# Performance work log

Measured on AMD Instinct MI355X. Metric: run time of the kernel, lower is better.

The kernel has to match this reference:

```python
import jax, jax.numpy as jnp
import numpy as np

HID, H, C, L = 128, 4, 128, 3  # hidden, heads, per-head out (concat=False -> mean over heads), layers
OUT = 256
N_HEX, N_VERT, N_EDGE, B = 19, 54, 72, 1024
F_HEX, F_VERT, F_EDGE, F_PLY = 9, 7, 5, 14


def _topology():
    # Deterministic stand-in for the Catan board topology (same edge counts as the env).
    rng = np.random.RandomState(0)
    hv = rng.randint(0, N_VERT, size=(N_HEX, 6))            # each hex touches 6 vertices
    v0 = rng.randint(0, N_VERT, size=N_EDGE)                # board-edge endpoints
    v1 = (v0 + 1 + rng.randint(0, N_VERT - 1, size=N_EDGE)) % N_VERT
    h_src = np.repeat(np.arange(N_HEX), 6); h_dst = hv.reshape(-1)           # 114 edges
    e_src = np.repeat(np.arange(N_EDGE), 2); e_dst = np.stack([v0, v1], 1).reshape(-1)  # 144
    vv_s = np.concatenate([v0, v1]); vv_d = np.concatenate([v1, v0])          # 144
    # (src_idx, dst_idx, n_dst) per relation, order matches RELATION_TYPES
    rels = [(h_src, h_dst, N_VERT),   # hex -> vertex
            (h_dst, h_src, N_HEX),    # vertex -> hex
            (e_dst, e_src, N_EDGE),   # vertex -> edge
            (e_src, e_dst, N_VERT),   # edge -> vertex
            (vv_s, vv_d, N_VERT)]     # vertex -> vertex
    return [(jnp.asarray(s, jnp.int32), jnp.asarray(d, jnp.int32), nd) for s, d, nd in rels]

RELS = _topology()
REL_TYPES = [("hex", "vertex"), ("vertex", "hex"), ("vertex", "edge"), ("edge", "vertex"), ("vertex", "vertex")]
NODE_TYPES = ("hex", "vertex", "edge")


def _gat(x_src, x_dst, W, a_s, a_d, b, src, dst, n_dst):
    """PyG GATConv (heads=H, concat=False, add_self_loops=False, shared lin)."""
    bsz = x_src.shape[0]
    g = (x_src @ W).reshape(bsz, -1, H, C)    # [B,Ns,H,C]
    gd = (x_dst @ W).reshape(bsz, -1, H, C)   # [B,Nd,H,C]
    es = jnp.einsum('bnhc,hc->bnh', g, a_s)
    ed = jnp.einsum('bnhc,hc->bnh', gd, a_d)
    e = jax.nn.leaky_relu(es[:, src] + ed[:, dst], 0.2)   # [B,E,H]
    e = jnp.transpose(e, (1, 0, 2))                       # [E,B,H]
    m = jax.ops.segment_max(e, dst, num_segments=n_dst)   # per-dst softmax
    ex = jnp.exp(e - m[dst])
    s = jax.ops.segment_sum(ex, dst, num_segments=n_dst)
    alpha = ex / (s[dst] + 1e-16)
    msg = jnp.transpose(g, (1, 0, 2, 3))[src] * alpha[..., None]   # [E,B,H,C]
    out = jax.ops.segment_sum(msg, dst, num_segments=n_dst)       # [Nd,B,H,C]
    return jnp.transpose(out.mean(axis=2), (1, 0, 2)) + b         # mean over heads, + bias


def _ln(x, g, b):
    mu = x.mean(-1, keepdims=True)
    var = ((x - mu) ** 2).mean(-1, keepdims=True)
    return (x - mu) / jnp.sqrt(var + 1e-5) * g + b


def setup_inputs() -> dict:
    key = jax.random.key(0)
    ks = jax.random.split(key, 20)
    rn = lambda k, shape, s=0.05: jax.random.normal(k, shape, jnp.float32) * s
    pool_dim = 3 * HID + F_PLY
    return {
        'hex_features': rn(ks[0], (B, N_HEX, F_HEX), 1.0),
        'vertex_features': rn(ks[1], (B, N_VERT, F_VERT), 1.0),
        'edge_features': rn(ks[2], (B, N_EDGE, F_EDGE), 1.0),
        'player_features': rn(ks[3], (B, 4, F_PLY), 1.0),
        'in_hexW': rn(ks[4], (F_HEX, HID)), 'in_hexb': jnp.zeros((HID,), jnp.float32),
        'in_vertW': rn(ks[5], (F_VERT, HID)), 'in_vertb': jnp.zeros((HID,), jnp.float32),
        'in_edgeW': rn(ks[6], (F_EDGE, HID)), 'in_edgeb': jnp.zeros((HID,), jnp.float32),
        'gat_W': rn(ks[7], (L, 5, HID, H * C)),
        'gat_asrc': rn(ks[8], (L, 5, H, C)),
        'gat_adst': rn(ks[9], (L, 5, H, C)),
        'gat_b': jnp.zeros((L, 5, C), jnp.float32),
        'ln_g': jnp.ones((L, 3, HID), jnp.float32),
        'ln_b': jnp.zeros((L, 3, HID), jnp.float32),
        'mlp_W1': rn(ks[10], (pool_dim, HID)), 'mlp_b1': jnp.zeros((HID,), jnp.float32),
        'mlp_W2': rn(ks[11], (HID, OUT)), 'mlp_b2': jnp.zeros((OUT,), jnp.float32),
        'current_player': jax.random.randint(ks[12], (B,), 0, 4, jnp.int32),
    }


def reference(hex_features, vertex_features, edge_features, player_features,
              in_hexW, in_hexb, in_vertW, in_vertb, in_edgeW, in_edgeb,
              gat_W, gat_asrc, gat_adst, gat_b, ln_g, ln_b,
              mlp_W1, mlp_b1, mlp_W2, mlp_b2, current_player):
    x = {'hex': hex_features @ in_hexW + in_hexb,
         'vertex': vertex_features @ in_vertW + in_vertb,
         'edge': edge_features @ in_edgeW + in_edgeb}
    for l in range(L):
        agg = {nt: jnp.zeros_like(x[nt]) for nt in NODE_TYPES}
        for r, (st, dt) in enumerate(REL_TYPES):
            src, dst, n_dst = RELS[r]
            agg[dt] = agg[dt] + _gat(x[st], x[dt], gat_W[l, r], gat_asrc[l, r],
                                     gat_adst[l, r], gat_b[l, r], src, dst, n_dst)
        for i, nt in enumerate(NODE_TYPES):
            x[nt] = jax.nn.relu(_ln(agg[nt] + x[nt], ln_g[l, i], ln_b[l, i]))
    pools = [x[nt].mean(axis=1) for nt in NODE_TYPES]  # mean-pool each node type
    cur = jnp.take_along_axis(player_features, current_player[:, None, None], axis=1)[:, 0]
    feat = jnp.concatenate(pools + [cur], axis=-1)     # [B, 3*HID + F_PLY]
    h = jax.nn.relu(feat @ mlp_W1 + mlp_b1)
    return h @ mlp_W2 + mlp_b2
```

## Files before the change

### kernel.cpp

```cpp
#include <hip/hip_runtime.h>
#include <math.h>

#define NB 1024
#define NHEX 19
#define NVERT 54
#define NEDGE 72
#define NNODE 145
#define HID 128
#define NLAYERS 3
#define MAXE 144
#define OUTD 256
#define FPLY 14
#define POOLD 398
#define ESD_PB 5120

typedef unsigned short ushort_t;
typedef short bf16x8 __attribute__((ext_vector_type(8)));
typedef float f32x4 __attribute__((ext_vector_type(4)));
typedef float f32x2 __attribute__((ext_vector_type(2)));

static __device__ __forceinline__ float bf2f(ushort_t u) {
    return __uint_as_float(((unsigned int)u) << 16);
}
static __device__ __forceinline__ ushort_t f2bf(float f) {
    unsigned int u = __float_as_uint(f);
    return (ushort_t)((u + 0x7fffu + ((u >> 16) & 1u)) >> 16);
}
static __device__ __forceinline__ unsigned pk2(float lo, float hi) {
    unsigned r;
    asm("v_cvt_pk_bf16_f32 %0, %1, %2" : "=v"(r) : "v"(lo), "v"(hi));
    return r;
}
static __device__ __forceinline__ float blo(unsigned u) { return __uint_as_float(u << 16); }
static __device__ __forceinline__ float bhi(unsigned u) { return __uint_as_float(u & 0xffff0000u); }
static __device__ __forceinline__ f32x4 MF(uint4 a, uint4 b, f32x4 c) {
    return __builtin_amdgcn_mfma_f32_16x16x32_bf16(
        __builtin_bit_cast(bf16x8, a), __builtin_bit_cast(bf16x8, b), c, 0, 0, 0);
}
static __device__ __forceinline__ int xba(int row, int cb) {
    return (row * 256 + cb) ^ ((row & 7) << 4);
}

__device__ __forceinline__ void topo_body(int* __restrict__ cst_g, unsigned* __restrict__ pck_g) {
    __shared__ unsigned mt[624];
    __shared__ int t6[624];
    __shared__ int sc[624];
    __shared__ int hv[114], v0a[72], v1a[72];
    __shared__ int cnt[80];
    __shared__ int dloc[73 * 24];
    __shared__ int J186;
    const int tid = threadIdx.x;

    if (tid == 0) {
        unsigned s = 0u;
        for (int i = 0; i < 624; ++i) { mt[i] = s; s = 1812433253u * (s ^ (s >> 30)) + (unsigned)i + 1u; }
    }
    __syncthreads();
    {
        unsigned a = 0, bb = 0, c = 0;
        if (tid < 227) { a = mt[tid]; bb = mt[tid + 1]; c = mt[tid + 397]; }
        __syncthreads();
        if (tid < 227) {
            unsigned y = (a & 0x80000000u) | (bb & 0x7fffffffu);
            mt[tid] = c ^ (y >> 1) ^ ((bb & 1u) ? 0x9908b0dfu : 0u);
        }
        __syncthreads();
    }
    {
        int i = 227 + tid;
        unsigned a = 0, bb = 0, c = 0;
        if (tid < 227) { a = mt[i]; bb = mt[i + 1]; c = mt[i - 227]; }
        __syncthreads();
        if (tid < 227) {
            unsigned y = (a & 0x80000000u) | (bb & 0x7fffffffu);
            mt[i] = c ^ (y >> 1) ^ ((bb & 1u) ? 0x9908b0dfu : 0u);
        }
        __syncthreads();
    }
    {
        int i = 454 + tid;
        unsigned a = 0, bb = 0, c = 0;
        if (tid < 170) { a = mt[i]; bb = mt[(i + 1) % 624]; c = mt[i - 227]; }
        __syncthreads();
        if (tid < 170) {
            unsigned y = (a & 0x80000000u) | (bb & 0x7fffffffu);
            mt[i] = c ^ (y >> 1) ^ ((bb & 1u) ? 0x9908b0dfu : 0u);
        }
        __syncthreads();
    }
    for (int i = tid; i < 624; i += 256) {
        unsigned y = mt[i];
        y ^= y >> 11; y ^= (y << 7) & 0x9d2c5680u; y ^= (y << 15) & 0xefc60000u; y ^= y >> 18;
        t6[i] = (int)(y & 63u);
    }
    __syncthreads();
#define SCAN624()                                                          \
    for (int off = 1; off < 624; off <<= 1) {                              \
        int v0_ = 0, v1_ = 0, v2_ = 0;                                     \
        int i0 = tid, i1 = tid + 256, i2 = tid + 512;                      \
        if (i0 >= off) v0_ = sc[i0 - off];                                 \
        if (i1 >= off) v1_ = sc[i1 - off];                                 \
        if (i2 < 624 && i2 >= off) v2_ = sc[i2 - off];                     \
        __syncthreads();                                                   \
        sc[i0] += v0_; sc[i1] += v1_;                                      \
        if (i2 < 624) sc[i2] += v2_;                                       \
        __syncthreads();                                                   \
    }
    for (int i = tid; i < 624; i += 256) sc[i] = (t6[i] <= 53) ? 1 : 0;
    __syncthreads();
    SCAN624();
    for (int i = tid; i < 624; i += 256) {
        if (t6[i] <= 53) {
            int k = sc[i];
            if (k <= 114) hv[k - 1] = t6[i];
            else if (k <= 186) v0a[k - 115] = t6[i];
            if (k == 186) J186 = i;
        }
    }
    __syncthreads();
    int Jcap = J186;
    for (int i = tid; i < 624; i += 256) sc[i] = (i > Jcap && t6[i] <= 52) ? 1 : 0;
    __syncthreads();
    SCAN624();
    for (int i = tid; i < 624; i += 256) {
        if (i > Jcap && t6[i] <= 52) {
            int k = sc[i];
            if (k <= 72) v1a[k - 1] = (v0a[k - 1] + 1 + t6[i]) % 54;
        }
    }
    __syncthreads();
#undef SCAN624
    const int En[5] = {114, 114, 144, 144, 144};
    const int Ndn[5] = {54, 19, 72, 54, 54};
    for (int r = 0; r < 5; ++r) {
        int E = En[r], Nd = Ndn[r];
        int myc = 0;
        if (tid < Nd) {
            int* ss = dloc + tid * 24;
            for (int k = 0; k < E; ++k) {
                int s, d;
                if (r == 0)      { s = k / 6; d = hv[k]; }
                else if (r == 1) { s = hv[k]; d = k / 6; }
                else if (r == 2) { s = (k & 1) ? v1a[k >> 1] : v0a[k >> 1]; d = k >> 1; }
                else if (r == 3) { s = k >> 1; d = (k & 1) ? v1a[k >> 1] : v0a[k >> 1]; }
                else             { s = (k < 72) ? v0a[k] : v1a[k - 72]; d = (k < 72) ? v1a[k] : v0a[k - 72]; }
                if (d != tid) continue;
                int f = -1;
                for (int i2 = 0; i2 < myc; ++i2) if ((ss[i2] & 255) == s) { f = i2; break; }
                if (f >= 0) ss[f] += 1 << 16;
                else { if (myc < 24) { ss[myc++] = s | (1 << 16); } }
            }
            cnt[tid] = myc;
        }
        __syncthreads();
        for (int off = 1; off < 128; off <<= 1) {
            int v = 0;
            if (tid < Nd && tid >= off) v = cnt[tid - off];
            __syncthreads();
            if (tid < Nd && tid >= off) cnt[tid] += v;
            __syncthreads();
        }
        if (tid < Nd) {
            int st = cnt[tid] - myc;
            cst_g[r * 73 + tid] = st;
            if (tid == Nd - 1) cst_g[r * 73 + Nd] = cnt[tid];
            int* ss = dloc + tid * 24;
            for (int i2 = 0; i2 < myc; ++i2)
                pck_g[r * 144 + st + i2] =
                    (unsigned)((ss[i2] & 255) | (tid << 8) | ((ss[i2] >> 16) << 16));
        }
        __syncthreads();
    }
}

__device__ __forceinline__ void wvec_body(int lr, const float* __restrict__ gat_W,
                                          const float* __restrict__ gat_asrc,
                                          const float* __restrict__ gat_adst,
                                          ushort_t* __restrict__ wvb) {
    __shared__ float as_s[512], ad_s[512];
    int tid = threadIdx.x;
    for (int i = tid; i < 512; i += 256) {
        as_s[i] = gat_asrc[(size_t)lr * 512 + i];
        ad_s[i] = gat_adst[(size_t)lr * 512 + i];
    }
    __syncthreads();
    ushort_t* wb = wvb + (size_t)lr * 2048;
    const float* W = gat_W + (size_t)lr * 128 * 512;
    int t127 = tid & 127, rhalf = tid >> 7;
    int h = t127 >> 5, c4 = t127 & 31;
    for (int k0 = 0; k0 < 128; k0 += 2) {
        int k = k0 + rhalf;
        float4 wv4 = *(const float4*)(W + (size_t)k * 512 + h * 128 + c4 * 4);
        const float* a = as_s + h * 128 + c4 * 4;
        const float* dd = ad_s + h * 128 + c4 * 4;
        float pa = wv4.x * a[0] + wv4.y * a[1] + wv4.z * a[2] + wv4.w * a[3];
        float pd = wv4.x * dd[0] + wv4.y * dd[1] + wv4.z * dd[2] + wv4.w * dd[3];
        for (int m = 1; m < 32; m <<= 1) { pa += __shfl_xor(pa, m, 64); pd += __shfl_xor(pd, m, 64); }
        if (c4 == 0) {
            ushort_t pah = f2bf(pa), pdh = f2bf(pd);
            ushort_t pal = f2bf(pa - bf2f(pah)), pdl = f2bf(pd - bf2f(pdh));
            wb[h * 128 + k] = pah;        wb[(4 + h) * 128 + k] = pdh;
            wb[(8 + h) * 128 + k] = pal;  wb[(12 + h) * 128 + k] = pdl;
        }
    }
}

__device__ __forceinline__ void wp_body(int lrh, const float* __restrict__ gat_W, ushort_t* __restrict__ Wp) {
    __shared__ ushort_t tr[128 * 130];
    int lr = lrh >> 2, h = lrh & 3;
    const float* Wsrc = gat_W + (size_t)lr * 128 * 512 + h * 128;
    for (int i = threadIdx.x; i < 128 * 32; i += 256) {
        int k = i >> 5, q = i & 31;
        float4 v = *(const float4*)(Wsrc + (size_t)k * 512 + q * 4);
        int n = q * 4;
        tr[(n + 0) * 130 + k] = f2bf(v.x);
        tr[(n + 1) * 130 + k] = f2bf(v.y);
        tr[(n + 2) * 130 + k] = f2bf(v.z);
        tr[(n + 3) * 130 + k] = f2bf(v.w);
    }
    __syncthreads();
    ushort_t* dst = Wp + (size_t)lrh * 128 * 128;
    for (int i = threadIdx.x; i < 128 * 16; i += 256) {
        int n = i >> 4, q = i & 15;
        const ushort_t* s = tr + n * 130 + q * 8;
        uint4 o;
        o.x = (unsigned)s[0] | ((unsigned)s[1] << 16);
        o.y = (unsigned)s[2] | ((unsigned)s[3] << 16);
        o.z = (unsigned)s[4] | ((unsigned)s[5] << 16);
        o.w = (unsigned)s[6] | ((unsigned)s[7] << 16);
        *(uint4*)(dst + n * 128 + q * 8) = o;
    }
}

__device__ __forceinline__ void proj_body(int b, const float* __restrict__ hexf, const float* __restrict__ vertf,
                                          const float* __restrict__ edgef,
                                          const float* __restrict__ Wh, const float* __restrict__ bh,
                                          const float* __restrict__ Wv, const float* __restrict__ bv,
                                          const float* __restrict__ We, const float* __restrict__ be,
                                          ushort_t* __restrict__ xb) {
    __shared__ float Wl[(9 + 7 + 5) * 128];
    __shared__ float bl[3 * 128];
    int tid = threadIdx.x;
    for (int i = tid; i < 9 * 128; i += 256) Wl[i] = Wh[i];
    for (int i = tid; i < 7 * 128; i += 256) Wl[9 * 128 + i] = Wv[i];
    for (int i = tid; i < 5 * 128; i += 256) Wl[16 * 128 + i] = We[i];
    if (tid < 128) { bl[tid] = bh[tid]; bl[128 + tid] = bv[tid]; bl[256 + tid] = be[tid]; }
    __syncthreads();
    int c = tid & 127;
    for (int n = tid >> 7; n < NNODE; n += 2) {
        const float* f; const float* W; const float* bias; int K;
        if (n < NHEX)              { f = hexf  + ((size_t)b * NHEX  + n) * 9;                  W = Wl;            bias = bl;       K = 9; }
        else if (n < NHEX + NVERT) { f = vertf + ((size_t)b * NVERT + (n - NHEX)) * 7;         W = Wl + 9 * 128;  bias = bl + 128; K = 7; }
        else                       { f = edgef + ((size_t)b * NEDGE + (n - NHEX - NVERT)) * 5; W = Wl + 16 * 128; bias = bl + 256; K = 5; }
        float acc = bias[c];
        for (int k = 0; k < K; ++k) acc += f[k] * W[k * 128 + c];
        xb[((size_t)b * NNODE + n) * HID + c] = f2bf(acc);
    }
}

__global__ __launch_bounds__(256) void k_pre(
        int* __restrict__ cst_g, unsigned* __restrict__ pck_g,
        const float* __restrict__ gatW, const float* __restrict__ gatas,
        const float* __restrict__ gatad, ushort_t* __restrict__ wvb, ushort_t* __restrict__ Wp,
        const float* __restrict__ hexf, const float* __restrict__ vertf, const float* __restrict__ edgef,
        const float* __restrict__ Wh, const float* __restrict__ bh,
        const float* __restrict__ Wv, const float* __restrict__ bv,
        const float* __restrict__ We, const float* __restrict__ be,
        ushort_t* __restrict__ xb) {
    unsigned kb = blockIdx.x;
    if (kb == 0)       topo_body(cst_g, pck_g);
    else if (kb < 16)  wvec_body((int)kb - 1, gatW, gatas, gatad, wvb);
    else if (kb < 76)  wp_body((int)kb - 16, gatW, Wp);
    else               proj_body((int)kb - 76, hexf, vertf, edgef, Wh, bh, Wv, bv, We, be, xb);
}

__global__ __launch_bounds__(256, 2) void k_logits0(const ushort_t* __restrict__ xb,
        const ushort_t* __restrict__ wvb, float* __restrict__ esd_g) {
    __shared__ __align__(16) char smem[NNODE * 256];
    int b = blockIdx.x, tid = threadIdx.x, lane = tid & 63, wid = tid >> 6;
    const int kc16 = (lane >> 4) * 16;
    const ushort_t* xcb = xb + (size_t)b * NNODE * HID;
    for (int i = tid; i < NNODE * 16; i += 256) {
        int row = i >> 4, q = i & 15;
        uint4 o = *(const uint4*)(xcb + (size_t)row * HID + q * 8);
        *(uint4*)(smem + xba(row, q * 16)) = o;
    }
    __syncthreads();
    const int NsA[5] = {19, 54, 54, 72, 54}, SbA[5] = {0, 19, 19, 73, 19};
    const int NdA[5] = {54, 19, 72, 54, 54}, DbA[5] = {19, 0, 73, 19, 19};
    for (int r = 0; r < 5; ++r) {
        int Ns = NsA[r];
        int RL = (r == 4) ? 54 : Ns + NdA[r];
        const ushort_t* wv = wvb + (size_t)r * 2048;
        uint4 bw[4];
#pragma unroll
        for (int ks = 0; ks < 4; ++ks)
            bw[ks] = *(const uint4*)(wv + (lane & 15) * 128 + ks * 32 + (lane >> 4) * 8);
        int T = (RL + 15) >> 4;
        for (int t = wid; t < T; t += 4) {
            int vrow = t * 16 + (lane & 15);
            int node = vrow < Ns ? SbA[r] + vrow : (vrow < RL ? DbA[r] + (vrow - Ns) : SbA[r]);
            f32x4 e = (f32x4){0.f, 0.f, 0.f, 0.f};
#pragma unroll
            for (int ks = 0; ks < 4; ++ks)
                e = MF(*(const uint4*)(smem + xba(node, ks * 64 + kc16)), bw[ks], e);
#pragma unroll
            for (int g = 0; g < 4; ++g) {
                float sv = e[g] + __shfl_xor(e[g], 8, 64);
                int row = t * 16 + (lane >> 4) * 4 + g;
                if ((lane & 15) < 8 && row < RL)
                    esd_g[(size_t)b * ESD_PB + r * 1024 + row * 8 + (lane & 15)] = sv;
            }
        }
    }
}

template<int KIND>
__device__ __forceinline__ void gnn_body(char* smem, int b,
        const ushort_t* __restrict__ xb_cur, ushort_t* __restrict__ xb_nxt,
        const float* __restrict__ esd_cur, float* __restrict__ esd_nxt,
        const int* __restrict__ cst_all, const unsigned* __restrict__ pck_all,
        const ushort_t* __restrict__ wvb, const ushort_t* __restrict__ Wp_g,
        const float* __restrict__ gatb_g,
        const float* __restrict__ lg, const float* __restrict__ lb, int l) {
    constexpr int ND    = (KIND == 0 ? 19 : KIND == 1 ? 72 : 54);
    constexpr int DB    = (KIND == 0 ? 0 : KIND == 1 ? 73 : 19);
    constexpr int NSMAX = (KIND == 2 ? 72 : 54);
    constexpr int NRELF = (KIND == 2 ? 3 : 1);
    constexpr int MT    = (ND + 15) / 16;
    constexpr int O_Y   = NSMAX * 256;
    constexpr int O_ESD = O_Y + ND * 256;
    constexpr int O_AL  = O_ESD + 4064;
    constexpr int O_CST = O_AL + 2304;
    constexpr int O_PCK = O_CST + 304;

    constexpr int NS_A[3][3] = {{54, 0, 0}, {54, 0, 0}, {19, 72, 54}};
    constexpr int SB_A[3][3] = {{19, 0, 0}, {19, 0, 0}, {0, 73, 19}};
    constexpr int RR_A[3][3] = {{1, 0, 0}, {2, 0, 0}, {0, 3, 4}};
    constexpr int NRE = (KIND == 2 ? 5 : 2);
    constexpr int RE_R[3][5] = {{0, 1, 0, 0, 0}, {2, 3, 0, 0, 0}, {0, 1, 2, 3, 4}};
    constexpr int RE_B[3][5] = {{0, 54, 0, 0, 0}, {54, 0, 0, 0, 0}, {19, 0, 0, 72, 0}};

    float*    esdL = (float*)(smem + O_ESD);
    float*    alph = (float*)(smem + O_AL);
    int*      cstL = (int*)(smem + O_CST);
    unsigned* pckL = (unsigned*)(smem + O_PCK);

    const int tid = threadIdx.x, lane = tid & 63, wid = tid >> 6;
    const int nr0 = wid * 32 + (lane & 15);
    const int kc16 = (lane >> 4) * 16;
    const ushort_t* xcb = xb_cur + (size_t)b * NNODE * HID;

    f32x4 acc[MT][2];
#pragma unroll
    for (int mt = 0; mt < MT; ++mt) {
        acc[mt][0] = (f32x4){0.f, 0.f, 0.f, 0.f};
        acc[mt][1] = (f32x4){0.f, 0.f, 0.f, 0.f};
    }

#pragma unroll
    for (int ri = 0; ri < NRELF; ++ri) {
        const int NS = NS_A[KIND][ri], SBG = SB_A[KIND][ri], r = RR_A[KIND][ri];
        const bool SELF = (KIND == 2 && ri == 2);
        const int lr = l * 5 + r;
        const int ER = SELF ? ND : NS + ND;

        for (int i = tid; i < NS * 16; i += 256) {
            int row = i >> 4, q = i & 15;
            uint4 o = *(const uint4*)(xcb + (size_t)(SBG + row) * HID + q * 8);
            *(uint4*)(smem + xba(row, q * 16)) = o;
        }
        {
            const float* eg = esd_cur + (size_t)b * ESD_PB + (size_t)r * 1024;
            for (int i = tid; i < ER * 2; i += 256)
                ((uint4*)esdL)[i] = ((const uint4*)eg)[i];
        }
        for (int i = tid; i <= ND; i += 256) cstL[i] = cst_all[r * 73 + i];
        for (int i = tid; i < 144; i += 256) pckL[i] = pck_all[r * 144 + i];
        __syncthreads();

        for (int i = tid; i < ND * 4; i += 256) {
            int d = i >> 2, h = i & 3;
            int s0 = cstL[d], s1 = cstL[d + 1];
            if (s0 == s1) continue;
            float edv = esdL[(SELF ? d : NS + d) * 8 + 4 + h];
            float m = -1e30f;
            for (int j = s0; j < s1; ++j) {
                float sv = esdL[(pckL[j] & 255) * 8 + h] + edv;
                sv = (sv >= 0.f) ? sv : 0.2f * sv;
                alph[j * 4 + h] = sv;
                m = fmaxf(m, sv);
            }
            float sum = 0.f;
            for (int j = s0; j < s1; ++j) {
                float e = (float)(pckL[j] >> 16) * __expf(alph[j * 4 + h] - m);
                alph[j * 4 + h] = e;
                sum += e;
            }
            float inv = 1.f / (sum + 1e-16f);
            for (int j = s0; j < s1; ++j) alph[j * 4 + h] *= inv;
        }
        __syncthreads();

        for (int h = 0; h < 4; ++h) {
            for (int i = tid; i < ND * 16; i += 256) {
                int d = i >> 4, c8 = i & 15;
                int s0 = cstL[d], s1 = cstL[d + 1];
                f32x2 a01 = (f32x2){0.f, 0.f}, a23 = (f32x2){0.f, 0.f};
                f32x2 a45 = (f32x2){0.f, 0.f}, a67 = (f32x2){0.f, 0.f};
                for (int j = s0; j < s1; ++j) {
                    float al = alph[j * 4 + h];
                    f32x2 al2 = (f32x2){al, al};
                    uint4 xv = *(const uint4*)(smem + xba((int)(pckL[j] & 255), c8 * 16));
                    a01 += al2 * (f32x2){blo(xv.x), bhi(xv.x)};
                    a23 += al2 * (f32x2){blo(xv.y), bhi(xv.y)};
                    a45 += al2 * (f32x2){blo(xv.z), bhi(xv.z)};
                    a67 += al2 * (f32x2){blo(xv.w), bhi(xv.w)};
                }
                uint4 o;
                o.x = pk2(a01[0], a01[1]); o.y = pk2(a23[0], a23[1]);
                o.z = pk2(a45[0], a45[1]); o.w = pk2(a67[0], a67[1]);
                *(uint4*)(smem + O_Y + xba(d, c8 * 16)) = o;
            }
            const ushort_t* wpH = Wp_g + (size_t)(lr * 4 + h) * 16384;
            __syncthreads();
#pragma unroll
            for (int ks = 0; ks < 4; ++ks) {
                uint4 b0 = *(const uint4*)(wpH + (size_t)nr0 * 128 + ks * 32 + (lane >> 4) * 8);
                uint4 b1 = *(const uint4*)(wpH + (size_t)(nr0 + 16) * 128 + ks * 32 + (lane >> 4) * 8);
#pragma unroll
                for (int mt = 0; mt < MT; ++mt) {
                    int arow = mt * 16 + (lane & 15);
                    if (arow >= ND) arow = ND - 1;
                    uint4 av = *(const uint4*)(smem + O_Y + xba(arow, ks * 64 + kc16));
                    acc[mt][0] = MF(av, b0, acc[mt][0]);
                    acc[mt][1] = MF(av, b1, acc[mt][1]);
                }
            }
            __syncthreads();
        }
    }

    float bn0 = 0.f, bn1 = 0.f;
#pragma unroll
    for (int ri = 0; ri < NRELF; ++ri) {
        const float* bb = gatb_g + (size_t)(l * 5 + RR_A[KIND][ri]) * 128;
        bn0 += bb[nr0]; bn1 += bb[nr0 + 16];
    }
    const float lgc0 = lg[nr0], lgc1 = lg[nr0 + 16];
    const float lbc0 = lb[nr0], lbc1 = lb[nr0 + 16];
#pragma unroll
    for (int mt = 0; mt < MT; ++mt)
#pragma unroll
        for (int g = 0; g < 4; ++g) {
            int row = mt * 16 + (lane >> 4) * 4 + g;
            if (row < ND) {
                acc[mt][0][g] = 0.25f * acc[mt][0][g] + bn0 + bf2f(xcb[(size_t)(DB + row) * HID + nr0]);
                acc[mt][1][g] = 0.25f * acc[mt][1][g] + bn1 + bf2f(xcb[(size_t)(DB + row) * HID + nr0 + 16]);
            }
        }
    float* red1 = esdL;
    float* red2 = esdL + 320;
#pragma unroll
    for (int mt = 0; mt < MT; ++mt)
#pragma unroll
        for (int g = 0; g < 4; ++g) {
            float p = acc[mt][0][g] + acc[mt][1][g];
            for (int m = 1; m < 16; m <<= 1) p += __shfl_xor(p, m, 64);
            int row = mt * 16 + (lane >> 4) * 4 + g;
            if ((lane & 15) == 0 && row < ND) red1[row * 4 + wid] = p;
        }
    __syncthreads();
    float mu[MT][4];
#pragma unroll
    for (int mt = 0; mt < MT; ++mt)
#pragma unroll
        for (int g = 0; g < 4; ++g) {
            int row = mt * 16 + (lane >> 4) * 4 + g;
            mu[mt][g] = 0.f;
            if (row < ND)
                mu[mt][g] = (red1[row * 4] + red1[row * 4 + 1] + red1[row * 4 + 2] + red1[row * 4 + 3]) * (1.f / 128.f);
            float d0 = acc[mt][0][g] - mu[mt][g], d1 = acc[mt][1][g] - mu[mt][g];
            float p = d0 * d0 + d1 * d1;
            for (int m = 1; m < 16; m <<= 1) p += __shfl_xor(p, m, 64);
            if ((lane & 15) == 0 && row < ND) red2[row * 4 + wid] = p;
        }
    __syncthreads();
#pragma unroll
    for (int mt = 0; mt < MT; ++mt)
#pragma unroll
        for (int g = 0; g < 4; ++g) {
            int row = mt * 16 + (lane >> 4) * 4 + g;
            if (row < ND) {
                float var = (red2[row * 4] + red2[row * 4 + 1] + red2[row * 4 + 2] + red2[row * 4 + 3]) * (1.f / 128.f);
                float rs = rsqrtf(var + 1e-5f);
                float o0 = fmaxf((acc[mt][0][g] - mu[mt][g]) * rs * lgc0 + lbc0, 0.f);
                float o1 = fmaxf((acc[mt][1][g] - mu[mt][g]) * rs * lgc1 + lbc1, 0.f);
                size_t gi = ((size_t)b * NNODE + DB + row) * HID;
                ushort_t u0 = f2bf(o0), u1 = f2bf(o1);
                xb_nxt[gi + nr0] = u0;
                xb_nxt[gi + nr0 + 16] = u1;
                if (esd_nxt) {
                    *(ushort_t*)(smem + O_Y + xba(row, nr0 * 2)) = u0;
                    *(ushort_t*)(smem + O_Y + xba(row, (nr0 + 16) * 2)) = u1;
                }
            }
        }
    if (esd_nxt) {
        __syncthreads();
        const int T = (ND + 15) >> 4;
        for (int t5 = wid; t5 < NRE * T; t5 += 4) {
            int e = t5 / T, tt = t5 % T;
            int r2 = RE_R[KIND][e], base = RE_B[KIND][e];
            const ushort_t* wv = wvb + (size_t)((l + 1) * 5 + r2) * 2048;
            uint4 bw[4];
#pragma unroll
            for (int ks = 0; ks < 4; ++ks)
                bw[ks] = *(const uint4*)(wv + (lane & 15) * 128 + ks * 32 + (lane >> 4) * 8);
            int arow = tt * 16 + (lane & 15);
            if (arow >= ND) arow = ND - 1;
            f32x4 ev = (f32x4){0.f, 0.f, 0.f, 0.f};
#pragma unroll
            for (int ks = 0; ks < 4; ++ks)
                ev = MF(*(const uint4*)(smem + O_Y + xba(arow, ks * 64 + kc16)), bw[ks], ev);
#pragma unroll
            for (int g = 0; g < 4; ++g) {
                float sv = ev[g] + __shfl_xor(ev[g], 8, 64);
                int row = tt * 16 + (lane >> 4) * 4 + g;
                if ((lane & 15) < 8 && row < ND)
                    esd_nxt[(size_t)b * ESD_PB + r2 * 1024 + (base + row) * 8 + (lane & 15)] = sv;
            }
        }
    }
}

#define SMEM_TOT 39504

__global__ __launch_bounds__(256, 3) void k_layer(
        const ushort_t* __restrict__ xb_cur, ushort_t* __restrict__ xb_nxt,
        const float* __restrict__ esd_cur, float* __restrict__ esd_nxt,
        const int* __restrict__ cst, const unsigned* __restrict__ pck,
        const ushort_t* __restrict__ wvb, const ushort_t* __restrict__ Wp,
        const float* __restrict__ gatb, const float* __restrict__ lngp,
        const float* __restrict__ lnbp, int l) {
    extern __shared__ uint4 smem_u4[];
    char* smem = (char*)smem_u4;
    unsigned kb = blockIdx.x;
    if (kb < NB)
        gnn_body<2>(smem, (int)kb, xb_cur, xb_nxt, esd_cur, esd_nxt, cst, pck, wvb, Wp, gatb,
                    lngp + (size_t)(l * 3 + 1) * 128, lnbp + (size_t)(l * 3 + 1) * 128, l);
    else if (kb < 2 * NB)
        gnn_body<1>(smem, (int)(kb - NB), xb_cur, xb_nxt, esd_cur, esd_nxt, cst, pck, wvb, Wp, gatb,
                    lngp + (size_t)(l * 3 + 2) * 128, lnbp + (size_t)(l * 3 + 2) * 128, l);
    else
        gnn_body<0>(smem, (int)(kb - 2 * NB), xb_cur, xb_nxt, esd_cur, esd_nxt, cst, pck, wvb, Wp, gatb,
                    lngp + (size_t)(l * 3 + 0) * 128, lnbp + (size_t)(l * 3 + 0) * 128, l);
}

__global__ __launch_bounds__(256) void k_head(const ushort_t* __restrict__ xb, const float* __restrict__ playerf,
                                              const int* __restrict__ curp,
                                              const float* __restrict__ W1, const float* __restrict__ b1,
                                              const float* __restrict__ W2, const float* __restrict__ b2,
                                              float* __restrict__ out) {
    __shared__ float fs[POOLD];
    __shared__ float ps[256];
    __shared__ float h1s[HID];
    int b = blockIdx.x, t = threadIdx.x;
    int c = t & 127, half = t >> 7;
    const ushort_t* xbb = xb + (size_t)b * NNODE * HID;
    float s0 = 0.f, s1 = 0.f, s2 = 0.f;
    for (int n = half; n < NHEX; n += 2)                    s0 += bf2f(xbb[n * HID + c]);
    for (int n = NHEX + half; n < NHEX + NVERT; n += 2)     s1 += bf2f(xbb[n * HID + c]);
    for (int n = NHEX + NVERT + half; n < NNODE; n += 2)    s2 += bf2f(xbb[n * HID + c]);
    ps[t] = s0; __syncthreads();
    if (half == 0) fs[c] = (ps[c] + ps[128 + c]) * (1.f / 19.f);
    __syncthreads(); ps[t] = s1; __syncthreads();
    if (half == 0) fs[128 + c] = (ps[c] + ps[128 + c]) * (1.f / 54.f);
    __syncthreads(); ps[t] = s2; __syncthreads();
    if (half == 0) fs[256 + c] = (ps[c] + ps[128 + c]) * (1.f / 72.f);
    if (t < FPLY) fs[384 + t] = playerf[((size_t)b * 4 + curp[b]) * FPLY + t];
    __syncthreads();
    float a = 0.f;
    int k0 = half * 199, k1 = half ? POOLD : 199;
    for (int k = k0; k < k1; ++k) a += fs[k] * W1[(size_t)k * HID + c];
    ps[t] = a; __syncthreads();
    if (half == 0) h1s[c] = fmaxf(b1[c] + ps[c] + ps[128 + c], 0.f);
    __syncthreads();
    float o = b2[t];
    for (int j = 0; j < HID; ++j) o += h1s[j] * W2[(size_t)j * OUTD + t];
    out[(size_t)b * OUTD + t] = o;
}

static constexpr size_t alignUp(size_t v) { return (v + 255) & ~(size_t)255; }
static constexpr size_t OFF_CST  = 0;
static constexpr size_t OFF_PCK  = alignUp(OFF_CST + 5 * 73 * 4);
static constexpr size_t OFF_WVB  = alignUp(OFF_PCK + 5 * 144 * 4);
static constexpr size_t OFF_WP   = alignUp(OFF_WVB + (size_t)15 * 16 * 128 * 2);
static constexpr size_t OFF_XA   = alignUp(OFF_WP + (size_t)15 * 4 * 128 * 128 * 2);
static constexpr size_t OFF_XB2  = alignUp(OFF_XA + (size_t)NB * NNODE * HID * 2);
static constexpr size_t OFF_ESD0 = alignUp(OFF_XB2 + (size_t)NB * NNODE * HID * 2);
static constexpr size_t OFF_ESD1 = alignUp(OFF_ESD0 + (size_t)NB * ESD_PB * 4);

extern "C" void kernel_launch(void* const* d_in, const int* in_sizes, int n_in,
                              void* d_out, int out_size, void* d_ws, size_t ws_size,
                              hipStream_t stream) {
    (void)in_sizes; (void)n_in; (void)out_size; (void)ws_size;
    const float* hexf   = (const float*)d_in[0];
    const float* vertf  = (const float*)d_in[1];
    const float* edgef  = (const float*)d_in[2];
    const float* playerf= (const float*)d_in[3];
    const float* inhW   = (const float*)d_in[4];
    const float* inhb   = (const float*)d_in[5];
    const float* invW   = (const float*)d_in[6];
    const float* invb   = (const float*)d_in[7];
    const float* ineW   = (const float*)d_in[8];
    const float* ineb   = (const float*)d_in[9];
    const float* gatW   = (const float*)d_in[10];
    const float* gatas  = (const float*)d_in[11];
    const float* gatad  = (const float*)d_in[12];
    const float* gatb   = (const float*)d_in[13];
    const float* lngp   = (const float*)d_in[14];
    const float* lnbp   = (const float*)d_in[15];
    const float* mW1    = (const float*)d_in[16];
    const float* mb1    = (const float*)d_in[17];
    const float* mW2    = (const float*)d_in[18];
    const float* mb2    = (const float*)d_in[19];
    const int*   curp   = (const int*)d_in[20];
    float* out = (float*)d_out;

    char* ws = (char*)d_ws;
    int* cst        = (int*)(ws + OFF_CST);
    unsigned* pck   = (unsigned*)(ws + OFF_PCK);
    ushort_t* wvb   = (ushort_t*)(ws + OFF_WVB);
    ushort_t* Wp    = (ushort_t*)(ws + OFF_WP);
    ushort_t* xbA   = (ushort_t*)(ws + OFF_XA);
    ushort_t* xbB   = (ushort_t*)(ws + OFF_XB2);
    float* esd0     = (float*)(ws + OFF_ESD0);
    float* esd1     = (float*)(ws + OFF_ESD1);

    k_pre<<<76 + NB, 256, 0, stream>>>(cst, pck, gatW, gatas, gatad, wvb, Wp,
                                       hexf, vertf, edgef, inhW, inhb, invW, invb, ineW, ineb, xbA);
    k_logits0<<<NB, 256, 0, stream>>>(xbA, wvb, esd0);

    for (int l = 0; l < NLAYERS; ++l) {
        const ushort_t* cur = (l & 1) ? xbB : xbA;
        ushort_t* nxt = (l & 1) ? xbA : xbB;
        const float* ecur = (l & 1) ? esd1 : esd0;
        float* enxt = (l == 2) ? nullptr : ((l & 1) ? esd0 : esd1);
        k_layer<<<3 * NB, 256, SMEM_TOT, stream>>>(cur, nxt, ecur, enxt, cst, pck, wvb, Wp,
                                                   gatb, lngp, lnbp, l);
    }

    k_head<<<NB, 256, 0, stream>>>(xbB, playerf, curp, mW1, mb1, mW2, mb2, out);
}
```

Baseline: 880.9 us.

## Split edge-node GNN blocks into two halves to balance per-block work

```diff
diff --git a/kernel.cpp b/kernel.cpp
--- a/kernel.cpp
+++ b/kernel.cpp
@@ -316,15 +316,15 @@
 }
 
 template<int KIND>
-__device__ __forceinline__ void gnn_body(char* smem, int b,
+__device__ __forceinline__ void gnn_body(char* smem, int b, int half,
         const ushort_t* __restrict__ xb_cur, ushort_t* __restrict__ xb_nxt,
         const float* __restrict__ esd_cur, float* __restrict__ esd_nxt,
         const int* __restrict__ cst_all, const unsigned* __restrict__ pck_all,
         const ushort_t* __restrict__ wvb, const ushort_t* __restrict__ Wp_g,
         const float* __restrict__ gatb_g,
         const float* __restrict__ lg, const float* __restrict__ lb, int l) {
-    constexpr int ND    = (KIND == 0 ? 19 : KIND == 1 ? 72 : 54);
-    constexpr int DB    = (KIND == 0 ? 0 : KIND == 1 ? 73 : 19);
+    constexpr int ND    = (KIND == 0 ? 19 : KIND == 1 ? 36 : 54);
+    constexpr int DBASE = (KIND == 0 ? 0 : KIND == 1 ? 73 : 19);
     constexpr int NSMAX = (KIND == 2 ? 72 : 54);
     constexpr int NRELF = (KIND == 2 ? 3 : 1);
     constexpr int MT    = (ND + 15) / 16;
@@ -349,6 +349,8 @@
     const int tid = threadIdx.x, lane = tid & 63, wid = tid >> 6;
     const int nr0 = wid * 32 + (lane & 15);
     const int kc16 = (lane >> 4) * 16;
+    const int d0 = half * ND;
+    const int DB = DBASE + d0;
     const ushort_t* xcb = xb_cur + (size_t)b * NNODE * HID;
 
     f32x4 acc[MT][2];
@@ -364,6 +366,7 @@
         const bool SELF = (KIND == 2 && ri == 2);
         const int lr = l * 5 + r;
         const int ER = SELF ? ND : NS + ND;
+        const int jlo = cst_all[r * 73 + d0];
 
         for (int i = tid; i < NS * 16; i += 256) {
             int row = i >> 4, q = i & 15;
@@ -372,18 +375,21 @@
         }
         {
             const float* eg = esd_cur + (size_t)b * ESD_PB + (size_t)r * 1024;
-            for (int i = tid; i < ER * 2; i += 256)
-                ((uint4*)esdL)[i] = ((const uint4*)eg)[i];
-        }
-        for (int i = tid; i <= ND; i += 256) cstL[i] = cst_all[r * 73 + i];
-        for (int i = tid; i < 144; i += 256) pckL[i] = pck_all[r * 144 + i];
+            for (int i = tid; i < ER * 2; i += 256) {
+                int row = i >> 1;
+                int grow = (SELF || row < NS) ? row : row + d0;
+                ((uint4*)esdL)[i] = ((const uint4*)eg)[grow * 2 + (i & 1)];
+            }
+        }
+        for (int i = tid; i <= ND; i += 256) cstL[i] = cst_all[r * 73 + d0 + i] - jlo;
+        for (int i = tid; jlo + i < 144; i += 256) pckL[i] = pck_all[r * 144 + jlo + i];
         __syncthreads();
 
         for (int i = tid; i < ND * 4; i += 256) {
             int d = i >> 2, h = i & 3;
             int s0 = cstL[d], s1 = cstL[d + 1];
             if (s0 == s1) continue;
-            float edv = esdL[(SELF ? d : NS + d) * 8 + 4 + h];
+            float edv = esdL[((SELF ? d + d0 : NS + d)) * 8 + 4 + h];
             float m = -1e30f;
             for (int j = s0; j < s1; ++j) {
                 float sv = esdL[(pckL[j] & 255) * 8 + h] + edv;
@@ -471,17 +477,17 @@
             if ((lane & 15) == 0 && row < ND) red1[row * 4 + wid] = p;
         }
     __syncthreads();
-    float mu[MT][4];
 #pragma unroll
     for (int mt = 0; mt < MT; ++mt)
 #pragma unroll
         for (int g = 0; g < 4; ++g) {
             int row = mt * 16 + (lane >> 4) * 4 + g;
-            mu[mt][g] = 0.f;
+            float mu = 0.f;
             if (row < ND)
-                mu[mt][g] = (red1[row * 4] + red1[row * 4 + 1] + red1[row * 4 + 2] + red1[row * 4 + 3]) * (1.f / 128.f);
-            float d0 = acc[mt][0][g] - mu[mt][g], d1 = acc[mt][1][g] - mu[mt][g];
-            float p = d0 * d0 + d1 * d1;
+                mu = (red1[row * 4] + red1[row * 4 + 1] + red1[row * 4 + 2] + red1[row * 4 + 3]) * (1.f / 128.f);
+            acc[mt][0][g] -= mu;
+            acc[mt][1][g] -= mu;
+            float p = acc[mt][0][g] * acc[mt][0][g] + acc[mt][1][g] * acc[mt][1][g];
             for (int m = 1; m < 16; m <<= 1) p += __shfl_xor(p, m, 64);
             if ((lane & 15) == 0 && row < ND) red2[row * 4 + wid] = p;
         }
@@ -494,8 +500,8 @@
             if (row < ND) {
                 float var = (red2[row * 4] + red2[row * 4 + 1] + red2[row * 4 + 2] + red2[row * 4 + 3]) * (1.f / 128.f);
                 float rs = rsqrtf(var + 1e-5f);
-                float o0 = fmaxf((acc[mt][0][g] - mu[mt][g]) * rs * lgc0 + lbc0, 0.f);
-                float o1 = fmaxf((acc[mt][1][g] - mu[mt][g]) * rs * lgc1 + lbc1, 0.f);
+                float o0 = fmaxf(acc[mt][0][g] * rs * lgc0 + lbc0, 0.f);
+                float o1 = fmaxf(acc[mt][1][g] * rs * lgc1 + lbc1, 0.f);
                 size_t gi = ((size_t)b * NNODE + DB + row) * HID;
                 ushort_t u0 = f2bf(o0), u1 = f2bf(o1);
                 xb_nxt[gi + nr0] = u0;
@@ -511,7 +517,7 @@
         const int T = (ND + 15) >> 4;
         for (int t5 = wid; t5 < NRE * T; t5 += 4) {
             int e = t5 / T, tt = t5 % T;
-            int r2 = RE_R[KIND][e], base = RE_B[KIND][e];
+            int r2 = RE_R[KIND][e], base = RE_B[KIND][e] + d0;
             const ushort_t* wv = wvb + (size_t)((l + 1) * 5 + r2) * 2048;
             uint4 bw[4];
 #pragma unroll
@@ -547,13 +553,14 @@
     char* smem = (char*)smem_u4;
     unsigned kb = blockIdx.x;
     if (kb < NB)
-        gnn_body<2>(smem, (int)kb, xb_cur, xb_nxt, esd_cur, esd_nxt, cst, pck, wvb, Wp, gatb,
+        gnn_body<2>(smem, (int)kb, 0, xb_cur, xb_nxt, esd_cur, esd_nxt, cst, pck, wvb, Wp, gatb,
                     lngp + (size_t)(l * 3 + 1) * 128, lnbp + (size_t)(l * 3 + 1) * 128, l);
-    else if (kb < 2 * NB)
-        gnn_body<1>(smem, (int)(kb - NB), xb_cur, xb_nxt, esd_cur, esd_nxt, cst, pck, wvb, Wp, gatb,
+    else if (kb < 3 * NB) {
+        unsigned t = kb - NB;
+        gnn_body<1>(smem, (int)(t >> 1), (int)(t & 1), xb_cur, xb_nxt, esd_cur, esd_nxt, cst, pck, wvb, Wp, gatb,
                     lngp + (size_t)(l * 3 + 2) * 128, lnbp + (size_t)(l * 3 + 2) * 128, l);
-    else
-        gnn_body<0>(smem, (int)(kb - 2 * NB), xb_cur, xb_nxt, esd_cur, esd_nxt, cst, pck, wvb, Wp, gatb,
+    } else
+        gnn_body<0>(smem, (int)(kb - 3 * NB), 0, xb_cur, xb_nxt, esd_cur, esd_nxt, cst, pck, wvb, Wp, gatb,
                     lngp + (size_t)(l * 3 + 0) * 128, lnbp + (size_t)(l * 3 + 0) * 128, l);
 }
 
@@ -647,7 +654,7 @@
         ushort_t* nxt = (l & 1) ? xbA : xbB;
         const float* ecur = (l & 1) ? esd1 : esd0;
         float* enxt = (l == 2) ? nullptr : ((l & 1) ? esd0 : esd1);
-        k_layer<<<3 * NB, 256, SMEM_TOT, stream>>>(cur, nxt, ecur, enxt, cst, pck, wvb, Wp,
+        k_layer<<<4 * NB, 256, SMEM_TOT, stream>>>(cur, nxt, ecur, enxt, cst, pck, wvb, Wp,
                                                    gatb, lngp, lnbp, l);
     }
 
```

Measured after the change: 774.3 us. -12.1%, faster.
